# Kernel optimization log

Hardware: AMD Instinct MI355X
Metric: run time of the kernel (lower is better)

The kernel has to match this reference:

```python
import jax, jax.numpy as jnp
import numpy as np
import math

L = 16
F = 2
T = 2 ** 19  # hashmap size (power of two)
BASE_RES = 16
MAX_RES = 2048
GROWTH = math.exp((math.log(MAX_RES) - math.log(BASE_RES)) / (L - 1))
RESOLUTIONS = np.array([int(math.ceil(BASE_RES * GROWTH ** l)) for l in range(L)], dtype=np.float32)
PRIMES = np.array([1, 2654435761, 805459861], dtype=np.uint32)
# 8 corner offsets of a unit cube, ordered as in the torch module
OFFSETS = np.array([[0,0,0],[0,0,1],[0,1,0],[0,1,1],[1,0,0],[1,0,1],[1,1,0],[1,1,1]], dtype=np.int32)
BBOX_MIN, BBOX_MAX = -1.0, 1.0


def setup_inputs() -> dict:
    key = jax.random.key(0)
    k1, k2 = jax.random.split(key)
    N = 1_000_000
    # world-space positions uniformly inside the default bbox [-1, 1]^3
    positions = jax.random.uniform(k1, (N, 3), dtype=jnp.float32, minval=-1.0, maxval=1.0)
    # hash tables init: uniform(-1e-4, 1e-4), matching nn.init.uniform_
    hash_tables = jax.random.uniform(k2, (L, T, F), dtype=jnp.float32, minval=-1e-4, maxval=1e-4)
    return {"positions": positions, "hash_tables": hash_tables}


def _hash_grid_forward(positions, hash_tables):
    res = jnp.asarray(RESOLUTIONS)                      # [L]
    primes = jnp.asarray(PRIMES)                        # [3] uint32
    offsets = jnp.asarray(OFFSETS)                      # [8,3] int32

    normalized = (positions - BBOX_MIN) / (BBOX_MAX - BBOX_MIN + 1e-8)
    normalized = jnp.clip(normalized, 0.0, 1.0 - 1e-6)  # [N,3]
    scaled = normalized[:, None, :] * res[None, :, None]  # [N,L,3]
    floor_coords = jnp.floor(scaled).astype(jnp.int32)
    frac = scaled - floor_coords.astype(jnp.float32)      # [N,L,3]

    corners = floor_coords[:, :, None, :] + offsets[None, None, :, :]  # [N,L,8,3]
    # spatial hash: (x*p0 ^ y*p1 ^ z*p2) mod T; uint32 wrap-around is
    # equivalent to the int64 torch version modulo T since T | 2^32
    c = corners.astype(jnp.uint32)
    h = (c[..., 0] * primes[0]) ^ (c[..., 1] * primes[1]) ^ (c[..., 2] * primes[2])
    hash_idx = (h % jnp.uint32(T)).astype(jnp.int32)      # [N,L,8]

    level_off = (jnp.arange(L, dtype=jnp.int32) * T)[None, :, None]  # [1,L,1]
    flat_idx = level_off + hash_idx                        # [N,L,8]
    corner_feats = hash_tables.reshape(L * T, F)[flat_idx]  # [N,L,8,F]

    fx = frac[..., 0:1]  # [N,L,1]
    fy = frac[..., 1:2]
    fz = frac[..., 2:3]
    c00 = corner_feats[:, :, 0] * (1 - fz) + corner_feats[:, :, 1] * fz
    c01 = corner_feats[:, :, 2] * (1 - fz) + corner_feats[:, :, 3] * fz
    c10 = corner_feats[:, :, 4] * (1 - fz) + corner_feats[:, :, 5] * fz
    c11 = corner_feats[:, :, 6] * (1 - fz) + corner_feats[:, :, 7] * fz
    c0 = c00 * (1 - fy) + c01 * fy
    c1 = c10 * (1 - fy) + c11 * fy
    out = c0 * (1 - fx) + c1 * fx                          # [N,L,F]
    return out.reshape(positions.shape[0], L * F)


def reference(positions, hash_tables):
    return _hash_grid_forward(positions, hash_tables)
```

## Files before the change

### kernel.cpp

```cpp
#include <hip/hip_runtime.h>
#include <math.h>

#define NUM_LEVELS 16
#define T_SIZE (1u << 19)
#define T_MASK (T_SIZE - 1u)
#define PRIME1 2654435761u
#define PRIME2 805459861u

struct ResParams { float r[NUM_LEVELS]; };

typedef float f32x2 __attribute__((ext_vector_type(2)));
typedef float f32x4 __attribute__((ext_vector_type(4)));

__device__ __forceinline__ void nt_store_f2(float2 v, float2* p) {
    f32x2 x; x.x = v.x; x.y = v.y;
    __builtin_nontemporal_store(x, (f32x2*)p);
}
__device__ __forceinline__ float2 nt_load_f2(const float2* p) {
    f32x2 x = __builtin_nontemporal_load((const f32x2*)p);
    float2 r; r.x = x.x; r.y = x.y; return r;
}
__device__ __forceinline__ void nt_store_f4(f32x4 v, float* p) {
    __builtin_nontemporal_store(v, (f32x4*)p);
}
__device__ __forceinline__ f32x4 nt_load_f4(const float* p) {
    return __builtin_nontemporal_load((const f32x4*)p);
}

struct CornerSet {
    unsigned idx[8];
    float fx, fy, fz;
};

__device__ __forceinline__ void calc_corners(
    float px, float py, float pz, float res, unsigned base, CornerSet& cs)
{
    float nx = (px + 1.0f) * 0.5f;
    float ny = (py + 1.0f) * 0.5f;
    float nz = (pz + 1.0f) * 0.5f;
    const float HI = 0.999999f;
    nx = fminf(fmaxf(nx, 0.0f), HI);
    ny = fminf(fmaxf(ny, 0.0f), HI);
    nz = fminf(fmaxf(nz, 0.0f), HI);

    float sx = nx * res, sy = ny * res, sz = nz * res;
    float flx = floorf(sx), fly = floorf(sy), flz = floorf(sz);
    cs.fx = sx - flx; cs.fy = sy - fly; cs.fz = sz - flz;

    unsigned ux = (unsigned)(int)flx;
    unsigned uy = (unsigned)(int)fly;
    unsigned uz = (unsigned)(int)flz;

    unsigned hx0 = ux;            unsigned hx1 = ux + 1u;
    unsigned hy0 = uy * PRIME1;   unsigned hy1 = hy0 + PRIME1;
    unsigned hz0 = uz * PRIME2;   unsigned hz1 = hz0 + PRIME2;

    cs.idx[0] = base + ((hx0 ^ hy0 ^ hz0) & T_MASK);
    cs.idx[1] = base + ((hx0 ^ hy0 ^ hz1) & T_MASK);
    cs.idx[2] = base + ((hx0 ^ hy1 ^ hz0) & T_MASK);
    cs.idx[3] = base + ((hx0 ^ hy1 ^ hz1) & T_MASK);
    cs.idx[4] = base + ((hx1 ^ hy0 ^ hz0) & T_MASK);
    cs.idx[5] = base + ((hx1 ^ hy0 ^ hz1) & T_MASK);
    cs.idx[6] = base + ((hx1 ^ hy1 ^ hz0) & T_MASK);
    cs.idx[7] = base + ((hx1 ^ hy1 ^ hz1) & T_MASK);
}

__device__ __forceinline__ float2 trilerp(const float2 f[8], float fx, float fy, float fz)
{
    float omz = 1.0f - fz, omy = 1.0f - fy, omx = 1.0f - fx;
    float c00x = f[0].x * omz + f[1].x * fz;
    float c00y = f[0].y * omz + f[1].y * fz;
    float c01x = f[2].x * omz + f[3].x * fz;
    float c01y = f[2].y * omz + f[3].y * fz;
    float c10x = f[4].x * omz + f[5].x * fz;
    float c10y = f[4].y * omz + f[5].y * fz;
    float c11x = f[6].x * omz + f[7].x * fz;
    float c11y = f[6].y * omz + f[7].y * fz;
    float c0x = c00x * omy + c01x * fy;
    float c0y = c00y * omy + c01y * fy;
    float c1x = c10x * omy + c11x * fy;
    float c1y = c10y * omy + c11y * fy;
    float2 o;
    o.x = c0x * omx + c1x * fx;
    o.y = c0y * omx + c1y * fx;
    return o;
}

__global__ __launch_bounds__(256) void hashgrid_gather_kernel(
    const float* __restrict__ pos,
    const float2* __restrict__ table,
    float2* __restrict__ ws,
    ResParams rp, int N)
{
    int level = blockIdx.y;
    int t = threadIdx.x;
    int n0 = blockIdx.x * 512 + t;
    int n1 = n0 + 256;
    bool v0 = n0 < N;
    bool v1 = n1 < N;
    if (!v0) return;

    float res = rp.r[level];
    unsigned base = (unsigned)level * T_SIZE;

    float px0 = pos[3 * n0 + 0], py0 = pos[3 * n0 + 1], pz0 = pos[3 * n0 + 2];
    int m1 = v1 ? n1 : n0;
    float px1 = pos[3 * m1 + 0], py1 = pos[3 * m1 + 1], pz1 = pos[3 * m1 + 2];

    CornerSet c0, c1;
    calc_corners(px0, py0, pz0, res, base, c0);
    calc_corners(px1, py1, pz1, res, base, c1);

    float2 f0[8], f1[8];
#pragma unroll
    for (int i = 0; i < 8; ++i) f0[i] = table[c0.idx[i]];
#pragma unroll
    for (int i = 0; i < 8; ++i) f1[i] = table[c1.idx[i]];

    float2 o0 = trilerp(f0, c0.fx, c0.fy, c0.fz);
    float2 o1 = trilerp(f1, c1.fx, c1.fy, c1.fz);

    nt_store_f2(o0, &ws[(size_t)level * N + n0]);
    if (v1) nt_store_f2(o1, &ws[(size_t)level * N + n1]);
}

__global__ __launch_bounds__(256) void hashgrid_transpose_kernel(
    const float2* __restrict__ ws,
    float* __restrict__ out,
    int N)
{
    __shared__ float2 tile[NUM_LEVELS][257];
    int base = blockIdx.x * 256;
    int t = threadIdx.x;
    int rem = N - base;

#pragma unroll
    for (int i = 0; i < 8; ++i) {
        int g = i * 256 + t;
        int l = g >> 7;
        int k = g & 127;
        int p = 2 * k;
        if (p + 1 < rem) {
            f32x4 v = nt_load_f4((const float*)&ws[(size_t)l * N + base + p]);
            float2 a; a.x = v.x; a.y = v.y;
            float2 b; b.x = v.z; b.y = v.w;
            tile[l][p] = a;
            tile[l][p + 1] = b;
        } else if (p < rem) {
            tile[l][p] = nt_load_f2(&ws[(size_t)l * N + base + p]);
        }
    }
    __syncthreads();

#pragma unroll
    for (int i = 0; i < 8; ++i) {
        int g = i * 256 + t;
        int p = g >> 3;
        int m = g & 7;
        if (p < rem) {
            float2 a = tile[2 * m][p];
            float2 b = tile[2 * m + 1][p];
            f32x4 v; v.x = a.x; v.y = a.y; v.z = b.x; v.w = b.y;
            nt_store_f4(v, &out[((size_t)(base + p) * 32) + m * 4]);
        }
    }
}

__global__ __launch_bounds__(256) void hashgrid_fused_kernel(
    const float* __restrict__ pos,
    const float2* __restrict__ table,
    float2* __restrict__ out,
    ResParams rp, int N)
{
    int tid = blockIdx.x * blockDim.x + threadIdx.x;
    int n = tid >> 4;
    int l = tid & 15;
    if (n >= N) return;
    float px = pos[3 * n + 0], py = pos[3 * n + 1], pz = pos[3 * n + 2];
    CornerSet c;
    calc_corners(px, py, pz, rp.r[l], (unsigned)l * T_SIZE, c);
    float2 f[8];
#pragma unroll
    for (int i = 0; i < 8; ++i) f[i] = table[c.idx[i]];
    out[tid] = trilerp(f, c.fx, c.fy, c.fz);
}

extern "C" void kernel_launch(void* const* d_in, const int* in_sizes, int n_in,
                              void* d_out, int out_size, void* d_ws, size_t ws_size,
                              hipStream_t stream) {
    const float*  pos   = (const float*)d_in[0];
    const float2* table = (const float2*)d_in[1];
    int N = in_sizes[0] / 3;

    ResParams rp;
    double growth = exp((log(2048.0) - log(16.0)) / 15.0);
    for (int l = 0; l < NUM_LEVELS; ++l) {
        rp.r[l] = (float)ceil(16.0 * pow(growth, (double)l));
    }

    size_t ws_needed = (size_t)NUM_LEVELS * (size_t)N * sizeof(float2);
    if (ws_size >= ws_needed) {
        float2* ws = (float2*)d_ws;
        int chunks = (N + 511) / 512;
        dim3 grid(chunks, NUM_LEVELS);
        hashgrid_gather_kernel<<<grid, 256, 0, stream>>>(pos, table, ws, rp, N);
        int tblocks = (N + 255) / 256;
        hashgrid_transpose_kernel<<<tblocks, 256, 0, stream>>>(ws, (float*)d_out, N);
    } else {
        long long total = (long long)N * NUM_LEVELS;
        int grid = (int)((total + 255) / 256);
        hashgrid_fused_kernel<<<grid, 256, 0, stream>>>(pos, table, (float2*)d_out, rp, N);
    }
}
```

Measured before the change: 648.1 us.

## Pair x-adjacent corner loads into 16-byte reads and simplify untile pass

When the floor x coordinate is even, the corners at x and x+1 hash to neighbouring table slots, because x enters the hash unmultiplied. The gather therefore fetches each such pair with one 16-byte load and swaps halves by index parity, which halves the number of gather instructions for those points. Each thread now handles two adjacent points and writes them with a single 16-byte store. The shared-memory transpose is replaced by a direct per-thread untile kernel that reads two level rows and writes 16 bytes, removing LDS use and barriers but making the reads less coalesced. The parity branch adds divergence within a wavefront.

```diff
diff --git a/kernel.cpp b/kernel.cpp
--- a/kernel.cpp
+++ b/kernel.cpp
@@ -23,12 +23,10 @@
 __device__ __forceinline__ void nt_store_f4(f32x4 v, float* p) {
     __builtin_nontemporal_store(v, (f32x4*)p);
 }
-__device__ __forceinline__ f32x4 nt_load_f4(const float* p) {
-    return __builtin_nontemporal_load((const f32x4*)p);
-}
 
 struct CornerSet {
     unsigned idx[8];
+    unsigned ux;
     float fx, fy, fz;
 };
 
@@ -50,6 +48,7 @@
     unsigned ux = (unsigned)(int)flx;
     unsigned uy = (unsigned)(int)fly;
     unsigned uz = (unsigned)(int)flz;
+    cs.ux = ux;
 
     unsigned hx0 = ux;            unsigned hx1 = ux + 1u;
     unsigned hy0 = uy * PRIME1;   unsigned hy1 = hy0 + PRIME1;
@@ -63,6 +62,27 @@
     cs.idx[5] = base + ((hx1 ^ hy0 ^ hz1) & T_MASK);
     cs.idx[6] = base + ((hx1 ^ hy1 ^ hz0) & T_MASK);
     cs.idx[7] = base + ((hx1 ^ hy1 ^ hz1) & T_MASK);
+}
+
+__device__ __forceinline__ void load_feats(
+    const float2* __restrict__ table, const CornerSet& cs, float2 f[8])
+{
+    if ((cs.ux & 1u) == 0u) {
+        const f32x4* t4 = reinterpret_cast<const f32x4*>(table);
+#pragma unroll
+        for (int j = 0; j < 4; ++j) {
+            unsigned i0 = cs.idx[j];
+            f32x4 v = t4[i0 >> 1];
+            float2 lo; lo.x = v.x; lo.y = v.y;
+            float2 hi; hi.x = v.z; hi.y = v.w;
+            bool sw = (i0 & 1u) != 0u;
+            f[j]     = sw ? hi : lo;
+            f[4 + j] = sw ? lo : hi;
+        }
+    } else {
+#pragma unroll
+        for (int i = 0; i < 8; ++i) f[i] = table[cs.idx[i]];
+    }
 }
 
 __device__ __forceinline__ float2 trilerp(const float2 f[8], float fx, float fy, float fz)
@@ -94,8 +114,8 @@
 {
     int level = blockIdx.y;
     int t = threadIdx.x;
-    int n0 = blockIdx.x * 512 + t;
-    int n1 = n0 + 256;
+    int n0 = blockIdx.x * 512 + 2 * t;
+    int n1 = n0 + 1;
     bool v0 = n0 < N;
     bool v1 = n1 < N;
     if (!v0) return;
@@ -112,58 +132,34 @@
     calc_corners(px1, py1, pz1, res, base, c1);
 
     float2 f0[8], f1[8];
-#pragma unroll
-    for (int i = 0; i < 8; ++i) f0[i] = table[c0.idx[i]];
-#pragma unroll
-    for (int i = 0; i < 8; ++i) f1[i] = table[c1.idx[i]];
+    load_feats(table, c0, f0);
+    load_feats(table, c1, f1);
 
     float2 o0 = trilerp(f0, c0.fx, c0.fy, c0.fz);
     float2 o1 = trilerp(f1, c1.fx, c1.fy, c1.fz);
 
-    nt_store_f2(o0, &ws[(size_t)level * N + n0]);
-    if (v1) nt_store_f2(o1, &ws[(size_t)level * N + n1]);
-}
-
-__global__ __launch_bounds__(256) void hashgrid_transpose_kernel(
+    size_t w = (size_t)level * N + n0;
+    if (v1) {
+        f32x4 v; v.x = o0.x; v.y = o0.y; v.z = o1.x; v.w = o1.y;
+        nt_store_f4(v, (float*)&ws[w]);
+    } else {
+        nt_store_f2(o0, &ws[w]);
+    }
+}
+
+__global__ __launch_bounds__(256) void hashgrid_untile_kernel(
     const float2* __restrict__ ws,
     float* __restrict__ out,
     int N)
 {
-    __shared__ float2 tile[NUM_LEVELS][257];
-    int base = blockIdx.x * 256;
-    int t = threadIdx.x;
-    int rem = N - base;
-
-#pragma unroll
-    for (int i = 0; i < 8; ++i) {
-        int g = i * 256 + t;
-        int l = g >> 7;
-        int k = g & 127;
-        int p = 2 * k;
-        if (p + 1 < rem) {
-            f32x4 v = nt_load_f4((const float*)&ws[(size_t)l * N + base + p]);
-            float2 a; a.x = v.x; a.y = v.y;
-            float2 b; b.x = v.z; b.y = v.w;
-            tile[l][p] = a;
-            tile[l][p + 1] = b;
-        } else if (p < rem) {
-            tile[l][p] = nt_load_f2(&ws[(size_t)l * N + base + p]);
-        }
-    }
-    __syncthreads();
-
-#pragma unroll
-    for (int i = 0; i < 8; ++i) {
-        int g = i * 256 + t;
-        int p = g >> 3;
-        int m = g & 7;
-        if (p < rem) {
-            float2 a = tile[2 * m][p];
-            float2 b = tile[2 * m + 1][p];
-            f32x4 v; v.x = a.x; v.y = a.y; v.z = b.x; v.w = b.y;
-            nt_store_f4(v, &out[((size_t)(base + p) * 32) + m * 4]);
-        }
-    }
+    int g = blockIdx.x * 256 + threadIdx.x;
+    int p = g >> 3;
+    int m = g & 7;
+    if (p >= N) return;
+    float2 a = nt_load_f2(&ws[(size_t)(2 * m) * N + p]);
+    float2 b = nt_load_f2(&ws[(size_t)(2 * m + 1) * N + p]);
+    f32x4 v; v.x = a.x; v.y = a.y; v.z = b.x; v.w = b.y;
+    nt_store_f4(v, &out[(size_t)p * 32 + m * 4]);
 }
 
 __global__ __launch_bounds__(256) void hashgrid_fused_kernel(
@@ -180,8 +176,7 @@
     CornerSet c;
     calc_corners(px, py, pz, rp.r[l], (unsigned)l * T_SIZE, c);
     float2 f[8];
-#pragma unroll
-    for (int i = 0; i < 8; ++i) f[i] = table[c.idx[i]];
+    load_feats(table, c, f);
     out[tid] = trilerp(f, c.fx, c.fy, c.fz);
 }
 
@@ -204,8 +199,9 @@
         int chunks = (N + 511) / 512;
         dim3 grid(chunks, NUM_LEVELS);
         hashgrid_gather_kernel<<<grid, 256, 0, stream>>>(pos, table, ws, rp, N);
-        int tblocks = (N + 255) / 256;
-        hashgrid_transpose_kernel<<<tblocks, 256, 0, stream>>>(ws, (float*)d_out, N);
+        long long tthreads = (long long)N * 8;
+        int tblocks = (int)((tthreads + 255) / 256);
+        hashgrid_untile_kernel<<<tblocks, 256, 0, stream>>>(ws, (float*)d_out, N);
     } else {
         long long total = (long long)N * NUM_LEVELS;
         int grid = (int)((total + 255) / 256);
```

After: 564.2 us. 12.9% less time.
